# Optimization experiments

Measured on AMD Instinct MI355X. Metric: run time of the kernel, lower is better.

## Reference

```python
import jax, jax.numpy as jnp
import numpy as np

N_NODES = 50000
N_EDGES = 600000
N_GRAPHS = 512
D = 128          # in_channels == hidden_channels
L = 4            # num_layers (total GINConv count)
N_CLASSES = 10
BN_EPS = 1e-5


def setup_inputs() -> dict:
    key = jax.random.key(0)
    ks = jax.random.split(key, 12)
    x = jax.random.normal(ks[0], (N_NODES, D), dtype=jnp.float32)
    edge_index = jax.random.randint(ks[1], (2, N_EDGES), 0, N_NODES, dtype=jnp.int64)
    batch = jnp.sort(jax.random.randint(ks[2], (N_NODES,), 0, N_GRAPHS, dtype=jnp.int64))
    s = 1.0 / np.sqrt(D)
    W1 = jax.random.uniform(ks[3], (L, D, D), jnp.float32, -s, s)
    b1 = jax.random.uniform(ks[4], (L, D), jnp.float32, -s, s)
    W2 = jax.random.uniform(ks[5], (L, D, D), jnp.float32, -s, s)
    b2 = jax.random.uniform(ks[6], (L, D), jnp.float32, -s, s)
    eps = jnp.zeros((L,), jnp.float32)            # train_eps=True, init 0
    gamma = jnp.ones((L, D), jnp.float32)
    beta = jnp.zeros((L, D), jnp.float32)
    sl = 1.0 / np.sqrt(D * L)
    Wlin = jax.random.uniform(ks[7], (D * L, N_CLASSES), jnp.float32, -sl, sl)
    blin = jax.random.uniform(ks[8], (N_CLASSES,), jnp.float32, -sl, sl)
    return {"x": x, "edge_index": edge_index, "batch": batch,
            "W1": W1, "b1": b1, "W2": W2, "b2": b2, "eps": eps,
            "gamma": gamma, "beta": beta, "Wlin": Wlin, "blin": blin}


def reference(x, edge_index, batch, W1, b1, W2, b2, eps, gamma, beta, Wlin, blin):
    src, dst = edge_index[0], edge_index[1]
    h = x
    pools = []
    for l in range(L):
        # GINConv: sum-aggregate neighbor features at dst, add (1+eps)*self
        agg = jax.ops.segment_sum(h[src], dst, num_segments=N_NODES)
        z = (1.0 + eps[l]) * h + agg
        # 2-layer MLP
        z = jnp.maximum(z @ W1[l] + b1[l], 0.0) @ W2[l] + b2[l]
        # BatchNorm1d (training mode: batch stats, biased variance)
        mean = jnp.mean(z, axis=0)
        var = jnp.mean(jnp.square(z - mean), axis=0)
        z = (z - mean) * jax.lax.rsqrt(var + BN_EPS) * gamma[l] + beta[l]
        h = jnp.maximum(z, 0.0)
        # global_add_pool per graph
        pools.append(jax.ops.segment_sum(h, batch, num_segments=N_GRAPHS))
    x_cat = jnp.concatenate(pools, axis=1)  # [N_GRAPHS, D*L]
    return x_cat @ Wlin + blin              # dropout = identity (eval)
```

## Files before the change

kernel.cpp:

```cpp
#include <hip/hip_runtime.h>

#define N_NODES 50000
#define N_EDGES 600000
#define N_GRAPHS 512
#define DIM 128
#define NLAYERS 4
#define NCLASSES 10
#define KPD 132

typedef __attribute__((ext_vector_type(8))) short short8;
typedef __attribute__((ext_vector_type(4))) float f32x4;

union Frag { short8 s; uint4 u; };

__device__ inline unsigned short f2bf(float v) {
    union { float f; unsigned u; } c; c.f = v;
    unsigned u = c.u;
    u += 0x7FFFu + ((u >> 16) & 1u);
    return (unsigned short)(u >> 16);
}
__device__ inline float bf2f(unsigned short h) {
    union { float f; unsigned u; } c; c.u = ((unsigned)h) << 16;
    return c.f;
}
__device__ inline float bfu_lo(unsigned u) {
    union { float f; unsigned x; } c; c.x = u << 16; return c.f;
}
__device__ inline float bfu_hi(unsigned u) {
    union { float f; unsigned x; } c; c.x = u & 0xFFFF0000u; return c.f;
}
__device__ inline void addRow(float* acc, const uint4& v) {
    acc[0] += bfu_lo(v.x); acc[1] += bfu_hi(v.x);
    acc[2] += bfu_lo(v.y); acc[3] += bfu_hi(v.y);
    acc[4] += bfu_lo(v.z); acc[5] += bfu_hi(v.z);
    acc[6] += bfu_lo(v.w); acc[7] += bfu_hi(v.w);
}

__global__ __launch_bounds__(256) void hist_kernel(
    const int* __restrict__ dst, int* __restrict__ deg)
{
    int e = blockIdx.x * 256 + threadIdx.x;
    if (e >= N_EDGES) return;
    atomicAdd(&deg[dst[e]], 1);
}

__global__ __launch_bounds__(256) void scan1_kernel(
    const int* __restrict__ deg, int* __restrict__ bsum)
{
    __shared__ int red[256];
    int t = threadIdx.x;
    int i4 = blockIdx.x * 256 + t;
    int s = 0;
    if (i4 < 12500) {
        int4 v = ((const int4*)deg)[i4];
        s = v.x + v.y + v.z + v.w;
    }
    red[t] = s;
    __syncthreads();
    for (int off = 128; off > 0; off >>= 1) {
        if (t < off) red[t] += red[t + off];
        __syncthreads();
    }
    if (t == 0) bsum[blockIdx.x] = red[0];
}

__global__ __launch_bounds__(64) void scan2_kernel(int* __restrict__ bsum)
{
    __shared__ int sh[64];
    int t = threadIdx.x;
    sh[t] = (t < 49) ? bsum[t] : 0;
    __syncthreads();
    if (t == 0) {
        int run = 0;
        for (int i = 0; i < 49; i++) { int v = sh[i]; sh[i] = run; run += v; }
    }
    __syncthreads();
    if (t < 49) bsum[t] = sh[t];
}

__global__ __launch_bounds__(256) void scan3_kernel(
    const int* __restrict__ deg, const int* __restrict__ bsum,
    int* __restrict__ rowptr, int* __restrict__ cursor)
{
    __shared__ int red[256];
    int t = threadIdx.x;
    int i4 = blockIdx.x * 256 + t;
    int4 v = {0, 0, 0, 0};
    if (i4 < 12500) v = ((const int4*)deg)[i4];
    int s = v.x + v.y + v.z + v.w;
    red[t] = s;
    __syncthreads();
    for (int off = 1; off < 256; off <<= 1) {
        int val = (t >= off) ? red[t - off] : 0;
        __syncthreads();
        red[t] += val;
        __syncthreads();
    }
    int run = bsum[blockIdx.x] + (t ? red[t - 1] : 0);
    if (i4 < 12500) {
        int4 rp;
        rp.x = run; run += v.x;
        rp.y = run; run += v.y;
        rp.z = run; run += v.z;
        rp.w = run; run += v.w;
        ((int4*)rowptr)[i4] = rp;
        ((int4*)cursor)[i4] = rp;
    }
    if (blockIdx.x == 0 && t == 0) rowptr[N_NODES] = N_EDGES;
}

__global__ __launch_bounds__(256) void fill_kernel(
    const int* __restrict__ src, const int* __restrict__ dst,
    int* __restrict__ cursor, int* __restrict__ csr)
{
    int e = blockIdx.x * 256 + threadIdx.x;
    if (e >= N_EDGES) return;
    int p = atomicAdd(&cursor[dst[e]], 1);
    csr[p] = src[e];
}

__global__ __launch_bounds__(256) void bounds_kernel(
    const int* __restrict__ batch, int* __restrict__ gstart)
{
    int n = blockIdx.x * 256 + threadIdx.x;
    if (n >= N_NODES) return;
    int b = batch[n];
    int bp = (n == 0) ? -1 : batch[n - 1];
    for (int g = bp + 1; g <= b; g++) gstart[g] = n;
    if (n == N_NODES - 1)
        for (int g = b + 1; g <= N_GRAPHS; g++) gstart[g] = N_NODES;
}

__global__ __launch_bounds__(256) void xconv_kernel(
    const float* __restrict__ x, unsigned int* __restrict__ xb)
{
    int idx = blockIdx.x * 256 + threadIdx.x;
    if (idx >= N_NODES * 32) return;
    float4 v = ((const float4*)x)[idx];
    uint2 o;
    o.x = (unsigned)f2bf(v.x) | ((unsigned)f2bf(v.y) << 16);
    o.y = (unsigned)f2bf(v.z) | ((unsigned)f2bf(v.w) << 16);
    ((uint2*)xb)[idx] = o;
}

__global__ __launch_bounds__(256) void wconv_kernel(
    const float* __restrict__ W1, const float* __restrict__ W2,
    unsigned short* __restrict__ whi)
{
    int idx = blockIdx.x * 256 + threadIdx.x;
    if (idx >= NLAYERS * 2 * 16384) return;
    int f   = idx & 16383;
    int w01 = (idx >> 14) & 1;
    int l   = idx >> 15;
    int j    = f & 7;
    int lane = (f >> 3) & 63;
    int cg   = (f >> 9) & 7;
    int ks   = f >> 12;
    int k = ks * 32 + (lane >> 4) * 8 + j;
    int n = cg * 16 + (lane & 15);
    const float* W = (w01 == 0 ? W1 : W2) + (size_t)l * 16384;
    whi[idx] = f2bf(W[k * 128 + n]);
}

__global__ __launch_bounds__(256) void gin_layer_kernel(
    const unsigned int* __restrict__ hb,
    const int* __restrict__ rowptr, const int* __restrict__ csr,
    const float* __restrict__ epsP,
    unsigned short* __restrict__ z,
    const unsigned short* __restrict__ whi,
    const float* __restrict__ b1, const float* __restrict__ b2,
    float* __restrict__ stats)
{
    __shared__ unsigned int tpk[64 * KPD];

    const int t = threadIdx.x;
    const int lane = t & 63;
    const int w = t >> 6;
    const int wr = w & 1, wc = w >> 1;
    const int l15 = lane & 15, quad = lane >> 4;
    const int base = blockIdx.x * 64;

    {
        const int m = t >> 2;
        const int c = t & 3;
        const int n = base + m;
        const uint4* hb4 = (const uint4*)hb;
        float acc[32];
        #pragma unroll
        for (int i = 0; i < 32; i++) acc[i] = 0.f;
        if (n < N_NODES) {
            const float e1 = 1.0f + epsP[0];
            const uint4* self = hb4 + (size_t)n * 16 + c * 4;
            #pragma unroll
            for (int j = 0; j < 4; j++) {
                uint4 v = self[j];
                float* a = acc + j * 8;
                a[0] = e1 * bfu_lo(v.x); a[1] = e1 * bfu_hi(v.x);
                a[2] = e1 * bfu_lo(v.y); a[3] = e1 * bfu_hi(v.y);
                a[4] = e1 * bfu_lo(v.z); a[5] = e1 * bfu_hi(v.z);
                a[6] = e1 * bfu_lo(v.w); a[7] = e1 * bfu_hi(v.w);
            }
            int beg = rowptr[n], end = rowptr[n + 1];
            int e = beg;
            for (; e + 3 < end; e += 4) {
                int s0 = csr[e], s1 = csr[e + 1], s2 = csr[e + 2], s3 = csr[e + 3];
                const uint4* r0 = hb4 + (size_t)s0 * 16 + c * 4;
                const uint4* r1 = hb4 + (size_t)s1 * 16 + c * 4;
                const uint4* r2 = hb4 + (size_t)s2 * 16 + c * 4;
                const uint4* r3 = hb4 + (size_t)s3 * 16 + c * 4;
                uint4 v00 = r0[0], v01 = r0[1], v02 = r0[2], v03 = r0[3];
                uint4 v10 = r1[0], v11 = r1[1], v12 = r1[2], v13 = r1[3];
                uint4 v20 = r2[0], v21 = r2[1], v22 = r2[2], v23 = r2[3];
                uint4 v30 = r3[0], v31 = r3[1], v32 = r3[2], v33 = r3[3];
                addRow(acc + 0, v00); addRow(acc + 8, v01); addRow(acc + 16, v02); addRow(acc + 24, v03);
                addRow(acc + 0, v10); addRow(acc + 8, v11); addRow(acc + 16, v12); addRow(acc + 24, v13);
                addRow(acc + 0, v20); addRow(acc + 8, v21); addRow(acc + 16, v22); addRow(acc + 24, v23);
                addRow(acc + 0, v30); addRow(acc + 8, v31); addRow(acc + 16, v32); addRow(acc + 24, v33);
            }
            for (; e < end; e++) {
                int s0 = csr[e];
                const uint4* r0 = hb4 + (size_t)s0 * 16 + c * 4;
                uint4 a0 = r0[0], a1 = r0[1], a2 = r0[2], a3 = r0[3];
                addRow(acc + 0, a0);  addRow(acc + 8, a1);
                addRow(acc + 16, a2); addRow(acc + 24, a3);
            }
        }
        uint4* dp = (uint4*)&tpk[m * KPD + c * 32];
        #pragma unroll
        for (int v4 = 0; v4 < 8; v4++) {
            uint4 pk;
            unsigned* pp = (unsigned*)&pk;
            #pragma unroll
            for (int j = 0; j < 4; j++) {
                float vv = acc[v4 * 4 + j];
                unsigned short h = f2bf(vv);
                unsigned short lo = f2bf(vv - bf2f(h));
                pp[j] = (unsigned)h | ((unsigned)lo << 16);
            }
            dp[v4] = pk;
        }
    }
    __syncthreads();

    f32x4 acc[2][4];
    #pragma unroll
    for (int s = 0; s < 2; s++)
        #pragma unroll
        for (int i = 0; i < 4; i++) acc[s][i] = (f32x4){0.f, 0.f, 0.f, 0.f};

    const int arowd0 = (32 * wr + l15) * KPD;
    const int arowd1 = arowd0 + 16 * KPD;

    #pragma unroll
    for (int kh = 0; kh < 2; kh++) {
        Frag bf[2][4];
        uint4 u00[2], u01[2], u10[2], u11[2];
        #pragma unroll
        for (int kk = 0; kk < 2; kk++) {
            int ks = kh * 2 + kk;
            #pragma unroll
            for (int i = 0; i < 4; i++) {
                size_t woff = (size_t)(((ks * 8 + wc * 4 + i) * 64 + lane) * 8);
                bf[kk][i].s = *((const short8*)&whi[woff]);
            }
            int kd = ks * 32 + quad * 8;
            u00[kk] = *((uint4*)&tpk[arowd0 + kd]);
            u01[kk] = *((uint4*)&tpk[arowd0 + kd + 4]);
            u10[kk] = *((uint4*)&tpk[arowd1 + kd]);
            u11[kk] = *((uint4*)&tpk[arowd1 + kd + 4]);
        }
        #pragma unroll
        for (int kk = 0; kk < 2; kk++) {
            Frag ah0, al0, ah1, al1;
            ah0.u = (uint4){ (u00[kk].x & 0xFFFFu) | (u00[kk].y << 16),
                             (u00[kk].z & 0xFFFFu) | (u00[kk].w << 16),
                             (u01[kk].x & 0xFFFFu) | (u01[kk].y << 16),
                             (u01[kk].z & 0xFFFFu) | (u01[kk].w << 16) };
            al0.u = (uint4){ (u00[kk].x >> 16) | (u00[kk].y & 0xFFFF0000u),
                             (u00[kk].z >> 16) | (u00[kk].w & 0xFFFF0000u),
                             (u01[kk].x >> 16) | (u01[kk].y & 0xFFFF0000u),
                             (u01[kk].z >> 16) | (u01[kk].w & 0xFFFF0000u) };
            ah1.u = (uint4){ (u10[kk].x & 0xFFFFu) | (u10[kk].y << 16),
                             (u10[kk].z & 0xFFFFu) | (u10[kk].w << 16),
                             (u11[kk].x & 0xFFFFu) | (u11[kk].y << 16),
                             (u11[kk].z & 0xFFFFu) | (u11[kk].w << 16) };
            al1.u = (uint4){ (u10[kk].x >> 16) | (u10[kk].y & 0xFFFF0000u),
                             (u10[kk].z >> 16) | (u10[kk].w & 0xFFFF0000u),
                             (u11[kk].x >> 16) | (u11[kk].y & 0xFFFF0000u),
                             (u11[kk].z >> 16) | (u11[kk].w & 0xFFFF0000u) };
            #pragma unroll
            for (int i = 0; i < 4; i++) {
                acc[0][i] = __builtin_amdgcn_mfma_f32_16x16x32_bf16(al0.s, bf[kk][i].s, acc[0][i], 0, 0, 0);
                acc[0][i] = __builtin_amdgcn_mfma_f32_16x16x32_bf16(ah0.s, bf[kk][i].s, acc[0][i], 0, 0, 0);
                acc[1][i] = __builtin_amdgcn_mfma_f32_16x16x32_bf16(al1.s, bf[kk][i].s, acc[1][i], 0, 0, 0);
                acc[1][i] = __builtin_amdgcn_mfma_f32_16x16x32_bf16(ah1.s, bf[kk][i].s, acc[1][i], 0, 0, 0);
            }
        }
    }
    __syncthreads();

    #pragma unroll
    for (int i = 0; i < 4; i++) {
        int col = wc * 64 + i * 16 + l15;
        float bb = b1[col];
        #pragma unroll
        for (int s = 0; s < 2; s++) {
            #pragma unroll
            for (int r = 0; r < 4; r++) {
                int m = 32 * wr + 16 * s + quad * 4 + r;
                float v = fmaxf(acc[s][i][r] + bb, 0.f);
                unsigned short h = f2bf(v);
                unsigned short lo2 = f2bf(v - bf2f(h));
                tpk[m * KPD + col] = (unsigned)h | ((unsigned)lo2 << 16);
            }
            acc[s][i] = (f32x4){0.f, 0.f, 0.f, 0.f};
        }
    }
    __syncthreads();

    const unsigned short* w2 = whi + 16384;
    #pragma unroll
    for (int kh = 0; kh < 2; kh++) {
        Frag bf[2][4];
        uint4 u00[2], u01[2], u10[2], u11[2];
        #pragma unroll
        for (int kk = 0; kk < 2; kk++) {
            int ks = kh * 2 + kk;
            #pragma unroll
            for (int i = 0; i < 4; i++) {
                size_t woff = (size_t)(((ks * 8 + wc * 4 + i) * 64 + lane) * 8);
                bf[kk][i].s = *((const short8*)&w2[woff]);
            }
            int kd = ks * 32 + quad * 8;
            u00[kk] = *((uint4*)&tpk[arowd0 + kd]);
            u01[kk] = *((uint4*)&tpk[arowd0 + kd + 4]);
            u10[kk] = *((uint4*)&tpk[arowd1 + kd]);
            u11[kk] = *((uint4*)&tpk[arowd1 + kd + 4]);
        }
        #pragma unroll
        for (int kk = 0; kk < 2; kk++) {
            Frag ah0, al0, ah1, al1;
            ah0.u = (uint4){ (u00[kk].x & 0xFFFFu) | (u00[kk].y << 16),
                             (u00[kk].z & 0xFFFFu) | (u00[kk].w << 16),
                             (u01[kk].x & 0xFFFFu) | (u01[kk].y << 16),
                             (u01[kk].z & 0xFFFFu) | (u01[kk].w << 16) };
            al0.u = (uint4){ (u00[kk].x >> 16) | (u00[kk].y & 0xFFFF0000u),
                             (u00[kk].z >> 16) | (u00[kk].w & 0xFFFF0000u),
                             (u01[kk].x >> 16) | (u01[kk].y & 0xFFFF0000u),
                             (u01[kk].z >> 16) | (u01[kk].w & 0xFFFF0000u) };
            ah1.u = (uint4){ (u10[kk].x & 0xFFFFu) | (u10[kk].y << 16),
                             (u10[kk].z & 0xFFFFu) | (u10[kk].w << 16),
                             (u11[kk].x & 0xFFFFu) | (u11[kk].y << 16),
                             (u11[kk].z & 0xFFFFu) | (u11[kk].w << 16) };
            al1.u = (uint4){ (u10[kk].x >> 16) | (u10[kk].y & 0xFFFF0000u),
                             (u10[kk].z >> 16) | (u10[kk].w & 0xFFFF0000u),
                             (u11[kk].x >> 16) | (u11[kk].y & 0xFFFF0000u),
                             (u11[kk].z >> 16) | (u11[kk].w & 0xFFFF0000u) };
            #pragma unroll
            for (int i = 0; i < 4; i++) {
                acc[0][i] = __builtin_amdgcn_mfma_f32_16x16x32_bf16(al0.s, bf[kk][i].s, acc[0][i], 0, 0, 0);
                acc[0][i] = __builtin_amdgcn_mfma_f32_16x16x32_bf16(ah0.s, bf[kk][i].s, acc[0][i], 0, 0, 0);
                acc[1][i] = __builtin_amdgcn_mfma_f32_16x16x32_bf16(al1.s, bf[kk][i].s, acc[1][i], 0, 0, 0);
                acc[1][i] = __builtin_amdgcn_mfma_f32_16x16x32_bf16(ah1.s, bf[kk][i].s, acc[1][i], 0, 0, 0);
            }
        }
    }
    __syncthreads();

    unsigned short* zs = (unsigned short*)tpk;
    float* sums = (float*)((char*)tpk + 20480);
    float* sqs  = sums + 1024;
    {
        float colsum[4], colsq[4];
        #pragma unroll
        for (int i = 0; i < 4; i++) {
            int col = wc * 64 + i * 16 + l15;
            float bb = b2[col];
            float su = 0.f, q2 = 0.f;
            #pragma unroll
            for (int s = 0; s < 2; s++) {
                #pragma unroll
                for (int r = 0; r < 4; r++) {
                    int m = 32 * wr + 16 * s + quad * 4 + r;
                    int n = base + m;
                    float v = acc[s][i][r] + bb;
                    zs[m * 136 + col] = f2bf(v);
                    if (n < N_NODES) { su += v; q2 += v * v; }
                }
            }
            colsum[i] = su; colsq[i] = q2;
        }
        #pragma unroll
        for (int i = 0; i < 4; i++) {
            sums[(w * 4 + i) * 64 + lane] = colsum[i];
            sqs [(w * 4 + i) * 64 + lane] = colsq[i];
        }
    }
    __syncthreads();

    {
        int m2 = t >> 2, c2 = t & 3;
        int n2 = base + m2;
        if (n2 < N_NODES) {
            const uint4* srcp = (const uint4*)(zs + m2 * 136 + c2 * 32);
            uint4* dstp = (uint4*)z + (size_t)n2 * 16 + c2 * 4;
            #pragma unroll
            for (int j = 0; j < 4; j++) dstp[j] = srcp[j];
        }
    }
    if (t < 128) {
        int c = t;
        int wcc = c >> 6, ci = (c >> 4) & 3, cl = c & 15;
        float s = 0.f, q2 = 0.f;
        #pragma unroll
        for (int wrr = 0; wrr < 2; wrr++) {
            int ww = wcc * 2 + wrr;
            #pragma unroll
            for (int u = 0; u < 4; u++) {
                int ln = cl + u * 16;
                s  += sums[(ww * 4 + ci) * 64 + ln];
                q2 += sqs [(ww * 4 + ci) * 64 + ln];
            }
        }
        unsafeAtomicAdd(&stats[c], s);
        unsafeAtomicAdd(&stats[128 + c], q2);
    }
}

__global__ __launch_bounds__(256) void bnpool_kernel(
    const unsigned int* __restrict__ z, const float* __restrict__ stats,
    const float* __restrict__ gamma, const float* __restrict__ beta,
    const int* __restrict__ gstart, unsigned int* __restrict__ hout,
    float* __restrict__ pools, int layer)
{
    __shared__ float red[8][128];
    const int g = blockIdx.x;
    const int t = threadIdx.x;
    const int q = t & 31, r = t >> 5;
    const int beg = gstart[g], end = gstart[g + 1];

    float4 s  = ((const float4*)stats)[q];
    float4 sq = ((const float4*)stats)[32 + q];
    float4 gm = ((const float4*)gamma)[q];
    float4 bt = ((const float4*)beta)[q];
    const float invN = 1.0f / (float)N_NODES;
    float m, vr;
    float4 scl, sh;
    m = s.x * invN; vr = sq.x * invN - m * m; scl.x = gm.x * rsqrtf(vr + 1e-5f); sh.x = bt.x - m * scl.x;
    m = s.y * invN; vr = sq.y * invN - m * m; scl.y = gm.y * rsqrtf(vr + 1e-5f); sh.y = bt.y - m * scl.y;
    m = s.z * invN; vr = sq.z * invN - m * m; scl.z = gm.z * rsqrtf(vr + 1e-5f); sh.z = bt.z - m * scl.z;
    m = s.w * invN; vr = sq.w * invN - m * m; scl.w = gm.w * rsqrtf(vr + 1e-5f); sh.w = bt.w - m * scl.w;

    float4 acc = {0.f, 0.f, 0.f, 0.f};
    for (int n = beg + r; n < end; n += 8) {
        uint2 zp = ((const uint2*)z)[(size_t)n * 32 + q];
        float4 hv;
        hv.x = fmaxf(bfu_lo(zp.x) * scl.x + sh.x, 0.f);
        hv.y = fmaxf(bfu_hi(zp.x) * scl.y + sh.y, 0.f);
        hv.z = fmaxf(bfu_lo(zp.y) * scl.z + sh.z, 0.f);
        hv.w = fmaxf(bfu_hi(zp.y) * scl.w + sh.w, 0.f);
        uint2 p;
        p.x = (unsigned)f2bf(hv.x) | ((unsigned)f2bf(hv.y) << 16);
        p.y = (unsigned)f2bf(hv.z) | ((unsigned)f2bf(hv.w) << 16);
        ((uint2*)hout)[(size_t)n * 32 + q] = p;
        acc.x += hv.x; acc.y += hv.y; acc.z += hv.z; acc.w += hv.w;
    }
    red[r][q * 4 + 0] = acc.x;
    red[r][q * 4 + 1] = acc.y;
    red[r][q * 4 + 2] = acc.z;
    red[r][q * 4 + 3] = acc.w;
    __syncthreads();
    if (t < 128) {
        float sm = 0.f;
        #pragma unroll
        for (int rr = 0; rr < 8; rr++) sm += red[rr][t];
        pools[(size_t)g * (DIM * NLAYERS) + (size_t)layer * DIM + t] = sm;
    }
}

__global__ __launch_bounds__(64) void final_kernel(
    const float* __restrict__ pools, const float* __restrict__ Wlin,
    const float* __restrict__ blin, float* __restrict__ out)
{
    int g = blockIdx.x;
    int lane = threadIdx.x;
    const float* xr = pools + (size_t)g * (DIM * NLAYERS);
    float a[NCLASSES];
    #pragma unroll
    for (int o = 0; o < NCLASSES; o++) a[o] = 0.f;
    for (int kk = 0; kk < DIM * NLAYERS; kk += 64) {
        float xv = xr[kk + lane];
        const float* wr = Wlin + (size_t)(kk + lane) * NCLASSES;
        #pragma unroll
        for (int o = 0; o < NCLASSES; o++) a[o] += xv * wr[o];
    }
    #pragma unroll
    for (int o = 0; o < NCLASSES; o++) {
        float v = a[o];
        #pragma unroll
        for (int off = 32; off > 0; off >>= 1) v += __shfl_down(v, off, 64);
        if (lane == 0) out[(size_t)g * NCLASSES + o] = v + blin[o];
    }
}

extern "C" void kernel_launch(void* const* d_in, const int* in_sizes, int n_in,
                              void* d_out, int out_size, void* d_ws, size_t ws_size,
                              hipStream_t stream)
{
    const float* x     = (const float*)d_in[0];
    const int*   src   = (const int*)d_in[1];
    const int*   dst   = ((const int*)d_in[1]) + N_EDGES;
    const int*   batch = (const int*)d_in[2];
    const float* W1    = (const float*)d_in[3];
    const float* b1    = (const float*)d_in[4];
    const float* W2    = (const float*)d_in[5];
    const float* b2    = (const float*)d_in[6];
    const float* eps   = (const float*)d_in[7];
    const float* gamma = (const float*)d_in[8];
    const float* beta  = (const float*)d_in[9];
    const float* Wlin  = (const float*)d_in[10];
    const float* blin  = (const float*)d_in[11];
    float* out = (float*)d_out;

    char* ws = (char*)d_ws;
    const size_t FEATH = (size_t)N_NODES * DIM * sizeof(unsigned short);
    size_t off = 0;
    unsigned int* buf_h = (unsigned int*)(ws + off); off += FEATH;
    unsigned short* buf_z = (unsigned short*)(ws + off); off += FEATH;
    float* pools  = (float*)(ws + off); off += (size_t)N_GRAPHS * DIM * NLAYERS * sizeof(float);
    float* stats  = (float*)(ws + off); off += (size_t)NLAYERS * 256 * sizeof(float);
    int*   deg    = (int*)(ws + off);   off += (size_t)N_NODES * sizeof(int);
    int*   rowptr = (int*)(ws + off);   off += (size_t)(N_NODES + 1) * sizeof(int) + 12;
    int*   csr    = (int*)(ws + off);   off += (size_t)N_EDGES * sizeof(int);
    int*   gstart = (int*)(ws + off);   off += 2064;
    int*   bsum   = (int*)(ws + off);   off += 208;
    unsigned short* whi = (unsigned short*)(ws + off); off += (size_t)NLAYERS * 2 * 16384 * 2;

    hipMemsetAsync(stats, 0, (size_t)NLAYERS * 256 * sizeof(float), stream);
    hipMemsetAsync(deg, 0, (size_t)N_NODES * sizeof(int), stream);

    hist_kernel<<<(N_EDGES + 255) / 256, 256, 0, stream>>>(dst, deg);
    scan1_kernel<<<49, 256, 0, stream>>>(deg, bsum);
    scan2_kernel<<<1, 64, 0, stream>>>(bsum);
    scan3_kernel<<<49, 256, 0, stream>>>(deg, bsum, rowptr, deg );
    fill_kernel<<<(N_EDGES + 255) / 256, 256, 0, stream>>>(src, dst, deg, csr);
    bounds_kernel<<<(N_NODES + 255) / 256, 256, 0, stream>>>(batch, gstart);
    xconv_kernel<<<(N_NODES * 32 + 255) / 256, 256, 0, stream>>>(x, buf_h);
    wconv_kernel<<<(NLAYERS * 2 * 16384 + 255) / 256, 256, 0, stream>>>(W1, W2, whi);

    for (int l = 0; l < NLAYERS; l++) {
        gin_layer_kernel<<<(N_NODES + 63) / 64, 256, 0, stream>>>(
            buf_h, rowptr, csr, eps + l, buf_z,
            whi + (size_t)l * 32768,
            b1 + (size_t)l * DIM, b2 + (size_t)l * DIM,
            stats + (size_t)l * 256);
        bnpool_kernel<<<N_GRAPHS, 256, 0, stream>>>(
            (const unsigned int*)buf_z, stats + (size_t)l * 256,
            gamma + (size_t)l * DIM, beta + (size_t)l * DIM,
            gstart, buf_h, pools, l);
    }
    final_kernel<<<N_GRAPHS, 64, 0, stream>>>(pools, Wlin, blin, out);
}
```

Before: 422.8 us.

## Sort nodes by in-degree so gather blocks get balanced work

Adds a degree histogram, a descending scan and a permutation kernel that group nodes by in-degree (capped at 63). The layer kernel then processes nodes in permuted order, so threads in a wave have similar neighbour counts and less divergence or tail imbalance in the sparse aggregation. This costs three extra setup kernels, an indirection through the permutation, scattered output writes, and atomic-ordered placement within each degree bucket, which loses node locality.

```diff
diff --git a/kernel.cpp b/kernel.cpp
--- a/kernel.cpp
+++ b/kernel.cpp
@@ -129,6 +129,42 @@
     for (int g = bp + 1; g <= b; g++) gstart[g] = n;
     if (n == N_NODES - 1)
         for (int g = b + 1; g <= N_GRAPHS; g++) gstart[g] = N_NODES;
+}
+
+__global__ __launch_bounds__(256) void dhist_kernel(
+    const int* __restrict__ rowptr, int* __restrict__ dhist)
+{
+    int n = blockIdx.x * 256 + threadIdx.x;
+    if (n >= N_NODES) return;
+    int d = rowptr[n + 1] - rowptr[n];
+    if (d > 63) d = 63;
+    atomicAdd(&dhist[d], 1);
+}
+
+__global__ __launch_bounds__(64) void dscan_kernel(int* __restrict__ dhist)
+{
+    __shared__ int sh[64];
+    int t = threadIdx.x;
+    sh[t] = dhist[t];
+    __syncthreads();
+    if (t == 0) {
+        int run = 0;
+        for (int b = 63; b >= 0; b--) { int v = sh[b]; sh[b] = run; run += v; }
+    }
+    __syncthreads();
+    dhist[t] = sh[t];
+}
+
+__global__ __launch_bounds__(256) void dperm_kernel(
+    const int* __restrict__ rowptr, int* __restrict__ dcur,
+    int* __restrict__ perm)
+{
+    int n = blockIdx.x * 256 + threadIdx.x;
+    if (n >= N_NODES) return;
+    int d = rowptr[n + 1] - rowptr[n];
+    if (d > 63) d = 63;
+    int pos = atomicAdd(&dcur[d], 1);
+    perm[pos] = n;
 }
 
 __global__ __launch_bounds__(256) void xconv_kernel(
@@ -165,6 +201,7 @@
 __global__ __launch_bounds__(256) void gin_layer_kernel(
     const unsigned int* __restrict__ hb,
     const int* __restrict__ rowptr, const int* __restrict__ csr,
+    const int* __restrict__ perm,
     const float* __restrict__ epsP,
     unsigned short* __restrict__ z,
     const unsigned short* __restrict__ whi,
@@ -172,6 +209,7 @@
     float* __restrict__ stats)
 {
     __shared__ unsigned int tpk[64 * KPD];
+    __shared__ int pm[64];
 
     const int t = threadIdx.x;
     const int lane = t & 63;
@@ -180,15 +218,22 @@
     const int l15 = lane & 15, quad = lane >> 4;
     const int base = blockIdx.x * 64;
 
+    if (t < 64) {
+        int slot = base + t;
+        pm[t] = (slot < N_NODES) ? perm[slot] : 0;
+    }
+    __syncthreads();
+
     {
         const int m = t >> 2;
         const int c = t & 3;
-        const int n = base + m;
+        const int slot = base + m;
+        const int n = pm[m];
         const uint4* hb4 = (const uint4*)hb;
         float acc[32];
         #pragma unroll
         for (int i = 0; i < 32; i++) acc[i] = 0.f;
-        if (n < N_NODES) {
+        if (slot < N_NODES) {
             const float e1 = 1.0f + epsP[0];
             const uint4* self = hb4 + (size_t)n * 16 + c * 4;
             #pragma unroll
@@ -382,10 +427,10 @@
                 #pragma unroll
                 for (int r = 0; r < 4; r++) {
                     int m = 32 * wr + 16 * s + quad * 4 + r;
-                    int n = base + m;
+                    int slot = base + m;
                     float v = acc[s][i][r] + bb;
                     zs[m * 136 + col] = f2bf(v);
-                    if (n < N_NODES) { su += v; q2 += v * v; }
+                    if (slot < N_NODES) { su += v; q2 += v * v; }
                 }
             }
             colsum[i] = su; colsq[i] = q2;
@@ -400,8 +445,9 @@
 
     {
         int m2 = t >> 2, c2 = t & 3;
-        int n2 = base + m2;
-        if (n2 < N_NODES) {
+        int slot = base + m2;
+        if (slot < N_NODES) {
+            int n2 = pm[m2];
             const uint4* srcp = (const uint4*)(zs + m2 * 136 + c2 * 32);
             uint4* dstp = (uint4*)z + (size_t)n2 * 16 + c2 * 4;
             #pragma unroll
@@ -534,23 +580,29 @@
     int*   csr    = (int*)(ws + off);   off += (size_t)N_EDGES * sizeof(int);
     int*   gstart = (int*)(ws + off);   off += 2064;
     int*   bsum   = (int*)(ws + off);   off += 208;
+    int*   dhist  = (int*)(ws + off);   off += 256;
+    int*   perm   = (int*)(ws + off);   off += (size_t)((N_NODES + 63) & ~63) * sizeof(int);
     unsigned short* whi = (unsigned short*)(ws + off); off += (size_t)NLAYERS * 2 * 16384 * 2;
 
     hipMemsetAsync(stats, 0, (size_t)NLAYERS * 256 * sizeof(float), stream);
     hipMemsetAsync(deg, 0, (size_t)N_NODES * sizeof(int), stream);
+    hipMemsetAsync(dhist, 0, 256, stream);
 
     hist_kernel<<<(N_EDGES + 255) / 256, 256, 0, stream>>>(dst, deg);
     scan1_kernel<<<49, 256, 0, stream>>>(deg, bsum);
     scan2_kernel<<<1, 64, 0, stream>>>(bsum);
     scan3_kernel<<<49, 256, 0, stream>>>(deg, bsum, rowptr, deg );
     fill_kernel<<<(N_EDGES + 255) / 256, 256, 0, stream>>>(src, dst, deg, csr);
+    dhist_kernel<<<(N_NODES + 255) / 256, 256, 0, stream>>>(rowptr, dhist);
+    dscan_kernel<<<1, 64, 0, stream>>>(dhist);
+    dperm_kernel<<<(N_NODES + 255) / 256, 256, 0, stream>>>(rowptr, dhist, perm);
     bounds_kernel<<<(N_NODES + 255) / 256, 256, 0, stream>>>(batch, gstart);
     xconv_kernel<<<(N_NODES * 32 + 255) / 256, 256, 0, stream>>>(x, buf_h);
     wconv_kernel<<<(NLAYERS * 2 * 16384 + 255) / 256, 256, 0, stream>>>(W1, W2, whi);
 
     for (int l = 0; l < NLAYERS; l++) {
         gin_layer_kernel<<<(N_NODES + 63) / 64, 256, 0, stream>>>(
-            buf_h, rowptr, csr, eps + l, buf_z,
+            buf_h, rowptr, csr, perm, eps + l, buf_z,
             whi + (size_t)l * 32768,
             b1 + (size_t)l * DIM, b2 + (size_t)l * DIM,
             stats + (size_t)l * 256);
```

After: 729.9 us. 1.73x slower.
